# Performance work log

Hardware: AMD Instinct MI355X
Metric: run time of the kernel (lower is better)

The kernel has to match this reference:

```python
import jax, jax.numpy as jnp
import numpy as np

BS = 4096
SEGLEN = 8192
LAMBDA1 = 8e-05  # smoothness weight
LAMBDA2 = 8e-05  # sparsity weight


def setup_inputs() -> dict:
    key = jax.random.key(0)
    k1, k2 = jax.random.split(key)
    scores = jax.random.uniform(k1, (BS, SEGLEN), dtype=jnp.float32)
    labels = jax.random.randint(k2, (BS,), 0, 2, dtype=jnp.int32)
    return {"scores": scores, "labels": labels}


def reference(scores, labels):
    # scores: [bs, seglen] float; labels: [bs] int (0 = normal, 1 = anomalous)
    pos = labels == 1
    neg = labels == 0

    # smooth(arr): cat([arr[1:], arr[-1:]]) - arr -> adjacent diffs, last term is 0
    d = scores[:, 1:] - scores[:, :-1]          # [bs, seglen-1]
    smooth = jnp.sum(d * d, axis=1)             # [bs]

    # sparsity(arr) (rtfm=False branch): plain sum
    spars = jnp.sum(scores, axis=1)             # [bs]

    # NOTE: original uses torch.max(scores, dim=1)[1] == ARGMAX INDICES (int64),
    # so the margin term is computed over integer indices, not max values.
    ms = jnp.argmax(scores, axis=1).astype(jnp.int32)  # [bs]

    # sum over j with labels[j]==0 of relu(1 - ms[i] + ms[j]), for each i
    pair = jnp.maximum(0, 1 - ms[:, None] + ms[None, :])        # [bs, bs] int32
    margin = jnp.sum(pair * neg[None, :].astype(jnp.int32), axis=1)  # [bs]

    per = LAMBDA1 * smooth + LAMBDA2 * spars + margin.astype(scores.dtype)
    L_sult = jnp.sum(jnp.where(pos, per, jnp.zeros_like(per))) / BS
    return L_sult
```

## Files before the change

### kernel.cpp

```cpp
#include <hip/hip_runtime.h>
#include <hip/hip_bf16.h>

#define BS      4096
#define SEGLEN  8192
#define LAMBDA1 8e-05f
#define LAMBDA2 8e-05f

__global__ __launch_bounds__(256) void row_stats(const float* __restrict__ scores,
                                                 float* __restrict__ smooth,
                                                 float* __restrict__ spars,
                                                 int*   __restrict__ ms) {
    const int row = blockIdx.x;
    const float* __restrict__ s = scores + (size_t)row * SEGLEN;
    const int t = threadIdx.x;

    float sum = 0.0f;
    float sq  = 0.0f;
    float mval = -1.0f;
    int   midx = SEGLEN;

    #pragma unroll
    for (int k = 0; k < SEGLEN / 4 / 256; ++k) {
        const int c4 = t + k * 256;
        const int c0 = c4 * 4;
        const float4 v = ((const float4*)s)[c4];
        const float nxt = (c0 + 4 < SEGLEN) ? s[c0 + 4] : v.w;

        const float d0 = v.y - v.x;
        const float d1 = v.z - v.y;
        const float d2 = v.w - v.z;
        const float d3 = nxt - v.w;
        sq  += d0 * d0 + d1 * d1 + d2 * d2 + d3 * d3;
        sum += v.x + v.y + v.z + v.w;

        if (v.x > mval) { mval = v.x; midx = c0;     }
        if (v.y > mval) { mval = v.y; midx = c0 + 1; }
        if (v.z > mval) { mval = v.z; midx = c0 + 2; }
        if (v.w > mval) { mval = v.w; midx = c0 + 3; }
    }

    #pragma unroll
    for (int off = 32; off > 0; off >>= 1) {
        sum += __shfl_xor(sum, off);
        sq  += __shfl_xor(sq,  off);
        const float ov = __shfl_xor(mval, off);
        const int   oi = __shfl_xor(midx, off);
        if (ov > mval || (ov == mval && oi < midx)) { mval = ov; midx = oi; }
    }

    __shared__ float ssum[4], ssq[4], smv[4];
    __shared__ int   smi[4];
    const int wave = t >> 6;
    if ((t & 63) == 0) { ssum[wave] = sum; ssq[wave] = sq; smv[wave] = mval; smi[wave] = midx; }
    __syncthreads();

    if (t == 0) {
        #pragma unroll
        for (int w = 1; w < 4; ++w) {
            sum += ssum[w];
            sq  += ssq[w];
            if (smv[w] > mval || (smv[w] == mval && smi[w] < midx)) { mval = smv[w]; midx = smi[w]; }
        }
        spars [row] = sum;
        smooth[row] = sq;
        ms    [row] = midx;
    }
}

__global__ __launch_bounds__(256) void margin_final(const float* __restrict__ smooth,
                                                    const float* __restrict__ spars,
                                                    const int*   __restrict__ ms,
                                                    const int*   __restrict__ labels,
                                                    float*       __restrict__ out) {
    const int i = blockIdx.x;
    if (labels[i] != 1) return;

    const int msi = ms[i];
    const int t = threadIdx.x;

    int acc = 0;
    for (int j = t; j < BS; j += 256) {
        if (labels[j] == 0) {
            const int v = 1 - msi + ms[j];
            acc += (v > 0) ? v : 0;
        }
    }

    #pragma unroll
    for (int off = 32; off > 0; off >>= 1)
        acc += __shfl_xor(acc, off);

    __shared__ int sacc[4];
    const int wave = t >> 6;
    if ((t & 63) == 0) sacc[wave] = acc;
    __syncthreads();

    if (t == 0) {
        acc += sacc[1] + sacc[2] + sacc[3];
        const float per = LAMBDA1 * smooth[i] + LAMBDA2 * spars[i] + (float)acc;
        atomicAdd(out, per * (1.0f / (float)BS));
    }
}

extern "C" void kernel_launch(void* const* d_in, const int* in_sizes, int n_in,
                              void* d_out, int out_size, void* d_ws, size_t ws_size,
                              hipStream_t stream) {
    const float* scores = (const float*)d_in[0];
    const int*   labels = (const int*)d_in[1];
    float*       out    = (float*)d_out;

    float* smooth = (float*)d_ws;
    float* spars  = smooth + BS;
    int*   ms     = (int*)(spars + BS);

    hipMemsetAsync(out, 0, sizeof(float), stream);

    row_stats<<<BS, 256, 0, stream>>>(scores, smooth, spars, ms);
    margin_final<<<BS, 256, 0, stream>>>(smooth, spars, ms, labels, out);
}
```

Baseline: 225.0 us.

## Batch margin rows per block with LDS-staged argmax and labels, drop memset

The margin kernel now runs 256 blocks, each staging all argmax indices and labels into shared memory and handling 16 rows, instead of one block per row. This cuts repeated global reads of ms/labels and reduces the number of atomics by combining the per-row terms into one partial per block. The output zeroing moves into row_stats, which removes the separate memset launch. It relies on stream ordering between the two kernels to guarantee the zeroing happens before the atomics. Parallelism drops to 256 blocks and the per-row integer sums are now accumulated in fewer threads.

```diff
diff --git a/kernel.cpp b/kernel.cpp
--- a/kernel.cpp
+++ b/kernel.cpp
@@ -9,10 +9,13 @@
 __global__ __launch_bounds__(256) void row_stats(const float* __restrict__ scores,
                                                  float* __restrict__ smooth,
                                                  float* __restrict__ spars,
-                                                 int*   __restrict__ ms) {
+                                                 int*   __restrict__ ms,
+                                                 float* __restrict__ out) {
     const int row = blockIdx.x;
     const float* __restrict__ s = scores + (size_t)row * SEGLEN;
     const int t = threadIdx.x;
+
+    if (row == 0 && t == 0) out[0] = 0.0f;
 
     float sum = 0.0f;
     float sq  = 0.0f;
@@ -67,38 +70,64 @@
     }
 }
 
+#define MB_BLOCKS 256
+#define IPB (BS / MB_BLOCKS)
+
 __global__ __launch_bounds__(256) void margin_final(const float* __restrict__ smooth,
                                                     const float* __restrict__ spars,
                                                     const int*   __restrict__ ms,
                                                     const int*   __restrict__ labels,
                                                     float*       __restrict__ out) {
-    const int i = blockIdx.x;
-    if (labels[i] != 1) return;
+    __shared__ int ms_l[BS];
+    __shared__ int lab_l[BS];
 
-    const int msi = ms[i];
     const int t = threadIdx.x;
+    const int b = blockIdx.x;
 
-    int acc = 0;
-    for (int j = t; j < BS; j += 256) {
-        if (labels[j] == 0) {
-            const int v = 1 - msi + ms[j];
-            acc += (v > 0) ? v : 0;
+    for (int idx = t; idx < BS; idx += 256) {
+        ms_l[idx]  = ms[idx];
+        lab_l[idx] = labels[idx];
+    }
+    __syncthreads();
+
+    int   macc = 0;
+    float facc = 0.0f;
+
+    #pragma unroll
+    for (int ii = 0; ii < IPB; ++ii) {
+        const int i = b * IPB + ii;
+        if (lab_l[i] == 1) {
+            const int base = 1 - ms_l[i];
+            for (int j = t; j < BS; j += 256) {
+                if (lab_l[j] == 0) {
+                    const int v = base + ms_l[j];
+                    macc += (v > 0) ? v : 0;
+                }
+            }
         }
+    }
+    if (t < IPB) {
+        const int i = b * IPB + t;
+        if (lab_l[i] == 1)
+            facc = LAMBDA1 * smooth[i] + LAMBDA2 * spars[i];
     }
 
     #pragma unroll
-    for (int off = 32; off > 0; off >>= 1)
-        acc += __shfl_xor(acc, off);
-
-    __shared__ int sacc[4];
+    for (int off = 32; off > 0; off >>= 1) {
+        macc += __shfl_xor(macc, off);
+        facc += __shfl_xor(facc, off);
+    }
+    __shared__ int   sacc[4];
+    __shared__ float sfac[4];
     const int wave = t >> 6;
-    if ((t & 63) == 0) sacc[wave] = acc;
+    if ((t & 63) == 0) { sacc[wave] = macc; sfac[wave] = facc; }
     __syncthreads();
 
     if (t == 0) {
-        acc += sacc[1] + sacc[2] + sacc[3];
-        const float per = LAMBDA1 * smooth[i] + LAMBDA2 * spars[i] + (float)acc;
-        atomicAdd(out, per * (1.0f / (float)BS));
+        macc += sacc[1] + sacc[2] + sacc[3];
+        facc += sfac[1] + sfac[2] + sfac[3];
+        const float partial = (facc + (float)macc) * (1.0f / (float)BS);
+        if (partial != 0.0f) atomicAdd(out, partial);
     }
 }
 
@@ -113,8 +142,6 @@
     float* spars  = smooth + BS;
     int*   ms     = (int*)(spars + BS);
 
-    hipMemsetAsync(out, 0, sizeof(float), stream);
-
-    row_stats<<<BS, 256, 0, stream>>>(scores, smooth, spars, ms);
-    margin_final<<<BS, 256, 0, stream>>>(smooth, spars, ms, labels, out);
+    row_stats<<<BS, 256, 0, stream>>>(scores, smooth, spars, ms, out);
+    margin_final<<<MB_BLOCKS, 256, 0, stream>>>(smooth, spars, ms, labels, out);
 }
```

Measured after the change: 214.9 us, median of 2. 4.5% less time.
